# Kernel tuning notes

Measured on AMD Instinct MI355X. Metric: run time of the kernel, lower is better.

Reference implementation:

```python
import jax, jax.numpy as jnp
import numpy as np

H = 16      # attention heads
D = 1024    # embedding size
HD = 64     # head size = D // H


def setup_inputs() -> dict:
    key = jax.random.key(0)
    ks = jax.random.split(key, 6)
    s = 1.0 / np.sqrt(D)
    x = jax.random.normal(ks[0], (2, 2048, D), dtype=jnp.float32)
    Wq = jax.random.normal(ks[1], (H, D, HD), dtype=jnp.float32) * s
    Wk = jax.random.normal(ks[2], (H, D, HD), dtype=jnp.float32) * s
    Wv = jax.random.normal(ks[3], (H, D, HD), dtype=jnp.float32) * s
    Wo = jax.random.normal(ks[4], (H * HD, D), dtype=jnp.float32) * s
    bo = jax.random.normal(ks[5], (D,), dtype=jnp.float32) * 0.01
    return {"x": x, "Wq": Wq, "Wk": Wk, "Wv": Wv, "Wo": Wo, "bo": bo}


def reference(x, Wq, Wk, Wv, Wo, bo):
    # x: [B, S, D]; per-head projections batched over the head axis.
    B, S, _ = x.shape
    q = jnp.einsum('bsd,hde->bhse', x, Wq)  # [B,H,S,HD]
    k = jnp.einsum('bsd,hde->bhse', x, Wk)
    v = jnp.einsum('bsd,hde->bhse', x, Wv)
    scale = 1.0 / jnp.sqrt(jnp.asarray(HD, dtype=x.dtype))
    scores = jnp.einsum('bhqe,bhke->bhqk', q, k) * scale  # [B,H,S,S]
    causal = jnp.tril(jnp.ones((S, S), dtype=bool))
    scores = jnp.where(causal, scores, jnp.asarray(-jnp.inf, dtype=x.dtype))
    attn = jax.nn.softmax(scores, axis=-1)
    out = jnp.einsum('bhqk,bhke->bhqe', attn, v)  # [B,H,S,HD]
    # concat heads along last dim (head order matches ModuleList order)
    out = out.transpose(0, 2, 1, 3).reshape(B, S, H * HD)
    return out @ Wo + bo  # dropout is identity in eval mode
```

## Files before the change

### kernel.cpp

```cpp
#include <hip/hip_runtime.h>
#include <hip/hip_bf16.h>
#include <cstdint>

#define Hh 16
#define Dd 1024
#define HD 64
#define Bb 2
#define Ss 2048

typedef float f32x4 __attribute__((ext_vector_type(4)));
typedef __bf16 bf16x8 __attribute__((ext_vector_type(8)));

__device__ __forceinline__ unsigned short f2bf(float f) {
  union { float f; unsigned u; } v; v.f = f;
  unsigned r = (v.u + 0x7FFFu + ((v.u >> 16) & 1u)) >> 16;
  return (unsigned short)r;
}

__device__ __forceinline__ void gld16(const void* g, void* l) {
  __builtin_amdgcn_global_load_lds(
      (__attribute__((address_space(1))) void*)(g),
      (__attribute__((address_space(3))) void*)(l),
      16, 0, 0);
}

__global__ __launch_bounds__(256)
void pack_x_k(const float4* __restrict__ x, unsigned short* __restrict__ xb, int n4) {
  const int i = blockIdx.x * blockDim.x + threadIdx.x;
  if (i >= n4) return;
  const float4 v = x[i];
  ushort4 o;
  o.x = f2bf(v.x); o.y = f2bf(v.y); o.z = f2bf(v.z); o.w = f2bf(v.w);
  *(ushort4*)&xb[(size_t)i * 4] = o;
}

__global__ __launch_bounds__(256)
void tconv_k(const float* __restrict__ in, unsigned short* __restrict__ out,
             int R, int C, float scale) {
  __shared__ float T[64][65];
  const int m = blockIdx.z;
  const float* src = in + (size_t)m * R * C;
  unsigned short* dst = out + (size_t)m * R * C;
  const int c0 = blockIdx.x * 64, r0 = blockIdx.y * 64;
  const int tx = threadIdx.x & 63, ty = threadIdx.x >> 6;
#pragma unroll
  for (int it = 0; it < 16; ++it) {
    const int i = ty + it * 4;
    T[i][tx] = src[(size_t)(r0 + i) * C + c0 + tx];
  }
  __syncthreads();
#pragma unroll
  for (int it = 0; it < 16; ++it) {
    const int jj = ty + it * 4;
    dst[(size_t)(c0 + jj) * R + r0 + tx] = f2bf(T[tx][jj] * scale);
  }
}

template <int EPI>
__global__ __launch_bounds__(256)
void gemm_bt(const unsigned short* __restrict__ A,
             const unsigned short* __restrict__ Bt,
             int K, int Ndim,
             unsigned short* __restrict__ q_out,
             unsigned short* __restrict__ k_out,
             unsigned short* __restrict__ vt_out,
             float* __restrict__ o_out,
             const float* __restrict__ bias)
{
  __shared__ unsigned short As[128 * 64];
  __shared__ unsigned short Bs[128 * 64];

  const int tid = threadIdx.x;
  const int w = tid >> 6, lane = tid & 63;
  const int lo = lane & 15, hi = lane >> 4;
  const int wr = w >> 1, wc = w & 1;
  const int row0 = blockIdx.y * 128;
  const int col0 = blockIdx.x * 128;

  f32x4 acc[4][4] = {};

  const int er = w * 32 + (lane >> 3);
  const int ec = (lane & 7) * 8;

  for (int k0 = 0; k0 < K; k0 += 64) {
#pragma unroll
    for (int c = 0; c < 4; ++c) {
      const int rr = er + c * 8;
      gld16(A  + (size_t)(row0 + rr) * K + (k0 + ec), (char*)As + (size_t)(w * 4 + c) * 1024);
      gld16(Bt + (size_t)(col0 + rr) * K + (k0 + ec), (char*)Bs + (size_t)(w * 4 + c) * 1024);
    }
    __syncthreads();
#pragma unroll
    for (int ks = 0; ks < 2; ++ks) {
      bf16x8 af[4], bfr[4];
#pragma unroll
      for (int i = 0; i < 4; ++i)
        af[i] = *(const bf16x8*)&As[(wr * 64 + i * 16 + lo) * 64 + ks * 32 + hi * 8];
#pragma unroll
      for (int j = 0; j < 4; ++j)
        bfr[j] = *(const bf16x8*)&Bs[(wc * 64 + j * 16 + lo) * 64 + ks * 32 + hi * 8];
#pragma unroll
      for (int i = 0; i < 4; ++i)
#pragma unroll
        for (int j = 0; j < 4; ++j)
          acc[i][j] = __builtin_amdgcn_mfma_f32_16x16x32_bf16(af[i], bfr[j], acc[i][j], 0, 0, 0);
    }
    __syncthreads();
  }

#pragma unroll
  for (int i = 0; i < 4; ++i) {
    const int grow = row0 + wr * 64 + i * 16 + hi * 4;
#pragma unroll
    for (int j = 0; j < 4; ++j) {
      const int gcol = col0 + wc * 64 + j * 16 + lo;
      if (EPI == 0) {
        const int p  = gcol >> 10;
        const int hd = (gcol >> 6) & 15;
        const int e  = gcol & 63;
        const int bb2 = grow >> 11;
        const int s   = grow & 2047;
        const int bh  = bb2 * Hh + hd;
        if (p == 2) {
          const size_t base = ((size_t)bh * HD + e) * Ss + s;
          ushort4 pk;
          pk.x = f2bf(acc[i][j][0]); pk.y = f2bf(acc[i][j][1]);
          pk.z = f2bf(acc[i][j][2]); pk.w = f2bf(acc[i][j][3]);
          *(ushort4*)&vt_out[base] = pk;
        } else {
          unsigned short* dst = (p == 0) ? q_out : k_out;
          const size_t base = ((size_t)bh * Ss + s) * HD + e;
#pragma unroll
          for (int r = 0; r < 4; ++r) dst[base + (size_t)r * HD] = f2bf(acc[i][j][r]);
        }
      } else {
        const size_t base = (size_t)grow * Ndim + gcol;
        const float bv = bias[gcol];
#pragma unroll
        for (int r = 0; r < 4; ++r) o_out[base + (size_t)r * Ndim] = acc[i][j][r] + bv;
      }
    }
  }
}

__global__ __launch_bounds__(256)
void attn_fwd(const unsigned short* __restrict__ qb,
              const unsigned short* __restrict__ kb,
              const unsigned short* __restrict__ vtb,
              unsigned short* __restrict__ ob)
{
  __shared__ unsigned short Ks[2][64 * 64];
  __shared__ unsigned short Vs[2][64 * 64];
  __shared__ unsigned short Ps[4][16 * 64];

  const int qt = 31 - blockIdx.y;
  const int bh = blockIdx.x;
  const int bb2 = bh >> 4;
  const int hd = bh & 15;

  const unsigned short* Q  = qb  + (size_t)bh * Ss * HD;
  const unsigned short* Kg = kb  + (size_t)bh * Ss * HD;
  const unsigned short* Vt = vtb + (size_t)bh * HD * Ss;

  const int tid = threadIdx.x;
  const int w = tid >> 6, lane = tid & 63;
  const int lo = lane & 15, hi = lane >> 4;
  const int qrow0 = qt * 64 + w * 16;

  const int srow = lane >> 3;
  const int scol = ((lane & 7) ^ (lane >> 3)) * 8;

#define STAGE(bi, kv)                                                     \
  _Pragma("unroll")                                                       \
  for (int c = 0; c < 2; ++c) {                                           \
    const int L = c * 4 + w;                                              \
    const int rr = L * 8 + srow;                                          \
    gld16(Kg + (size_t)((kv) + rr) * HD + scol,                           \
          (char*)&Ks[bi][0] + L * 1024);                                  \
    gld16(Vt + (size_t)rr * Ss + (kv) + scol,                             \
          (char*)&Vs[bi][0] + L * 1024);                                  \
  }

  const int swl = (lo & 7) << 4;

  bf16x8 vones;
#pragma unroll
  for (int j = 0; j < 8; ++j) vones[j] = (__bf16)1.0f;

  bf16x8 qf[2];
#pragma unroll
  for (int ks = 0; ks < 2; ++ks)
    qf[ks] = *(const bf16x8*)&Q[(size_t)(qrow0 + lo) * HD + ks * 32 + hi * 8];

  f32x4 oacc[4] = {};
  float m2[4], l2[4];
#pragma unroll
  for (int r = 0; r < 4; ++r) { m2[r] = -INFINITY; l2[r] = 0.f; }

  const int ntiles = qt + 1;

  STAGE(0, 0);
  __syncthreads();

  int cur = 0;
  for (int t = 0; t < ntiles; ++t) {
    if (t + 1 < ntiles) { STAGE(cur ^ 1, (t + 1) * 64); }

    const int kv0 = t * 64;
    const bool diag = (t == qt);

    f32x4 sacc[4] = {};
    __builtin_amdgcn_s_setprio(1);
#pragma unroll
    for (int ks = 0; ks < 2; ++ks) {
      bf16x8 kf[4];
#pragma unroll
      for (int nj = 0; nj < 4; ++nj)
        kf[nj] = *(const bf16x8*)((const char*)&Ks[cur][0] +
                 (nj * 16 + lo) * 128 + ((ks * 64 + hi * 16) ^ swl));
#pragma unroll
      for (int nj = 0; nj < 4; ++nj)
        sacc[nj] = __builtin_amdgcn_mfma_f32_16x16x32_bf16(qf[ks], kf[nj], sacc[nj], 0, 0, 0);
    }
    __builtin_amdgcn_s_setprio(0);

    float lm[4];
    float dmax = -INFINITY;
#pragma unroll
    for (int r = 0; r < 4; ++r) {
      if (diag) {
        const int q = qrow0 + hi * 4 + r;
#pragma unroll
        for (int nj = 0; nj < 4; ++nj) {
          const int kk = kv0 + nj * 16 + lo;
          if (kk > q) sacc[nj][r] = -INFINITY;
        }
      }
      lm[r] = fmaxf(fmaxf(sacc[0][r], sacc[1][r]), fmaxf(sacc[2][r], sacc[3][r]));
      dmax = fmaxf(dmax, lm[r] - m2[r]);
    }
    if (!__all(dmax <= 8.0f)) {
#pragma unroll
      for (int r = 0; r < 4; ++r) {
        float rm = lm[r];
#pragma unroll
        for (int d = 1; d < 16; d <<= 1)
          rm = fmaxf(rm, __shfl_xor(rm, d, 64));
        const float mn = fmaxf(m2[r], rm);
        const float rc = __builtin_amdgcn_exp2f(m2[r] - mn);
        m2[r] = mn;
        l2[r] *= rc;
#pragma unroll
        for (int nj = 0; nj < 4; ++nj)
          oacc[nj][r] *= rc;
      }
    }

    unsigned short* Pw = &Ps[w][0];
#pragma unroll
    for (int nj = 0; nj < 4; ++nj)
#pragma unroll
      for (int r = 0; r < 4; ++r) {
        const float p = __builtin_amdgcn_exp2f(sacc[nj][r] - m2[r]);
        const int prow = hi * 4 + r;
        const int pcb = (nj * 32 + lo * 2) ^ ((prow & 7) << 4);
        *(__bf16*)((char*)Pw + prow * 128 + pcb) = (__bf16)p;
      }

    f32x4 osum = {};
    __builtin_amdgcn_s_setprio(1);
#pragma unroll
    for (int ks = 0; ks < 2; ++ks) {
      bf16x8 pa, vf[4];
      pa = *(const bf16x8*)((const char*)Pw +
           lo * 128 + ((ks * 64 + hi * 16) ^ swl));
#pragma unroll
      for (int nj = 0; nj < 4; ++nj)
        vf[nj] = *(const bf16x8*)((const char*)&Vs[cur][0] +
                 (nj * 16 + lo) * 128 + ((ks * 64 + hi * 16) ^ swl));
#pragma unroll
      for (int nj = 0; nj < 4; ++nj)
        oacc[nj] = __builtin_amdgcn_mfma_f32_16x16x32_bf16(pa, vf[nj], oacc[nj], 0, 0, 0);
      osum = __builtin_amdgcn_mfma_f32_16x16x32_bf16(pa, vones, osum, 0, 0, 0);
    }
    __builtin_amdgcn_s_setprio(0);
#pragma unroll
    for (int r = 0; r < 4; ++r)
      l2[r] += osum[r];

    __syncthreads();
    cur ^= 1;
  }
#undef STAGE

#pragma unroll
  for (int r = 0; r < 4; ++r) {
    const int s = qrow0 + hi * 4 + r;
    const float il = 1.0f / l2[r];
    const size_t base = ((size_t)bb2 * Ss + s) * Dd + hd * HD;
#pragma unroll
    for (int nj = 0; nj < 4; ++nj)
      ob[base + nj * 16 + lo] = f2bf(oacc[nj][r] * il);
  }
}

extern "C" void kernel_launch(void* const* d_in, const int* in_sizes, int n_in,
                              void* d_out, int out_size, void* d_ws, size_t ws_size,
                              hipStream_t stream)
{
  const float* x  = (const float*)d_in[0];
  const float* Wq = (const float*)d_in[1];
  const float* Wk = (const float*)d_in[2];
  const float* Wv = (const float*)d_in[3];
  const float* Wo = (const float*)d_in[4];
  const float* bo = (const float*)d_in[5];
  float* out = (float*)d_out;

  char* ws = (char*)d_ws;
  unsigned short* xb    = (unsigned short*)(ws);
  unsigned short* wqkvT = (unsigned short*)(ws + 8388608);
  unsigned short* woT   = (unsigned short*)(ws + 14680064);
  unsigned short* qb    = (unsigned short*)(ws + 16777216);
  unsigned short* kb    = (unsigned short*)(ws + 25165824);
  unsigned short* vtb   = (unsigned short*)(ws + 33554432);
  unsigned short* ob    = (unsigned short*)(ws + 41943040);

  pack_x_k<<<4096, 256, 0, stream>>>((const float4*)x, xb, 1048576);
  tconv_k<<<dim3(1, 16, 16), 256, 0, stream>>>(Wq, wqkvT,           1024, 64, 0.18033688011112042f);
  tconv_k<<<dim3(1, 16, 16), 256, 0, stream>>>(Wk, wqkvT + 1048576, 1024, 64, 1.0f);
  tconv_k<<<dim3(1, 16, 16), 256, 0, stream>>>(Wv, wqkvT + 2097152, 1024, 64, 1.0f);
  tconv_k<<<dim3(16, 16, 1), 256, 0, stream>>>(Wo, woT,             1024, 1024, 1.0f);

  gemm_bt<0><<<dim3(24, 32), 256, 0, stream>>>(xb, wqkvT, 1024, 3072,
                                               qb, kb, vtb, nullptr, nullptr);
  attn_fwd<<<dim3(32, 32), 256, 0, stream>>>(qb, kb, vtb, ob);
  gemm_bt<1><<<dim3(8, 32), 256, 0, stream>>>(ob, woT, 1024, 1024,
                                              nullptr, nullptr, nullptr, out, bo);
}
```

Before: 140.3 us.

## Double-buffer GEMM LDS tiles with swizzle and vectorize transposed epilogue stores

The GEMM now double-buffers its A/B LDS tiles, issuing the next tile's async global-to-LDS loads before computing the current one. It adds an XOR swizzle to cut LDS bank conflicts and raises wave priority around the MFMA block. For Q/K and the output projection it swaps the MFMA operand order so each lane holds four consecutive columns, allowing packed ushort4/float4 stores instead of scalar strided stores. The V projection moves to its own launch that keeps the transposed layout, so the QKV GEMM becomes two kernels, and doubling LDS may lower occupancy.

```diff
diff --git a/kernel.cpp b/kernel.cpp
--- a/kernel.cpp
+++ b/kernel.cpp
@@ -67,8 +67,8 @@
              float* __restrict__ o_out,
              const float* __restrict__ bias)
 {
-  __shared__ unsigned short As[128 * 64];
-  __shared__ unsigned short Bs[128 * 64];
+  __shared__ unsigned short As[2][128 * 64];
+  __shared__ unsigned short Bs[2][128 * 64];
 
   const int tid = threadIdx.x;
   const int w = tid >> 6, lane = tid & 63;
@@ -79,68 +79,91 @@
 
   f32x4 acc[4][4] = {};
 
-  const int er = w * 32 + (lane >> 3);
-  const int ec = (lane & 7) * 8;
-
-  for (int k0 = 0; k0 < K; k0 += 64) {
-#pragma unroll
-    for (int c = 0; c < 4; ++c) {
-      const int rr = er + c * 8;
-      gld16(A  + (size_t)(row0 + rr) * K + (k0 + ec), (char*)As + (size_t)(w * 4 + c) * 1024);
-      gld16(Bt + (size_t)(col0 + rr) * K + (k0 + ec), (char*)Bs + (size_t)(w * 4 + c) * 1024);
-    }
-    __syncthreads();
+  const int srow = w * 32 + (lane >> 3);
+  const int scol = ((lane & 7) ^ (lane >> 3)) * 8;
+  const int swl  = (lo & 7) << 4;
+
+#define GSTAGE(bi, k0)                                                    \
+  _Pragma("unroll")                                                       \
+  for (int c = 0; c < 4; ++c) {                                           \
+    const int rr = srow + c * 8;                                          \
+    gld16(A  + (size_t)(row0 + rr) * K + ((k0) + scol),                   \
+          (char*)&As[bi][0] + (w * 4 + c) * 1024);                        \
+    gld16(Bt + (size_t)(col0 + rr) * K + ((k0) + scol),                   \
+          (char*)&Bs[bi][0] + (w * 4 + c) * 1024);                        \
+  }
+
+  GSTAGE(0, 0);
+  __syncthreads();
+
+  const int nst = K >> 6;
+  int cur = 0;
+  for (int t = 0; t < nst; ++t) {
+    if (t + 1 < nst) { GSTAGE(cur ^ 1, (t + 1) * 64); }
 #pragma unroll
     for (int ks = 0; ks < 2; ++ks) {
       bf16x8 af[4], bfr[4];
 #pragma unroll
       for (int i = 0; i < 4; ++i)
-        af[i] = *(const bf16x8*)&As[(wr * 64 + i * 16 + lo) * 64 + ks * 32 + hi * 8];
+        af[i] = *(const bf16x8*)((const char*)&As[cur][0] +
+                 (wr * 64 + i * 16 + lo) * 128 + ((ks * 64 + hi * 16) ^ swl));
 #pragma unroll
       for (int j = 0; j < 4; ++j)
-        bfr[j] = *(const bf16x8*)&Bs[(wc * 64 + j * 16 + lo) * 64 + ks * 32 + hi * 8];
+        bfr[j] = *(const bf16x8*)((const char*)&Bs[cur][0] +
+                 (wc * 64 + j * 16 + lo) * 128 + ((ks * 64 + hi * 16) ^ swl));
+      __builtin_amdgcn_s_setprio(1);
 #pragma unroll
       for (int i = 0; i < 4; ++i)
 #pragma unroll
-        for (int j = 0; j < 4; ++j)
-          acc[i][j] = __builtin_amdgcn_mfma_f32_16x16x32_bf16(af[i], bfr[j], acc[i][j], 0, 0, 0);
+        for (int j = 0; j < 4; ++j) {
+          if (EPI == 1)
+            acc[i][j] = __builtin_amdgcn_mfma_f32_16x16x32_bf16(af[i], bfr[j], acc[i][j], 0, 0, 0);
+          else
+            acc[i][j] = __builtin_amdgcn_mfma_f32_16x16x32_bf16(bfr[j], af[i], acc[i][j], 0, 0, 0);
+        }
+      __builtin_amdgcn_s_setprio(0);
     }
     __syncthreads();
+    cur ^= 1;
   }
 
 #pragma unroll
   for (int i = 0; i < 4; ++i) {
-    const int grow = row0 + wr * 64 + i * 16 + hi * 4;
 #pragma unroll
     for (int j = 0; j < 4; ++j) {
-      const int gcol = col0 + wc * 64 + j * 16 + lo;
-      if (EPI == 0) {
-        const int p  = gcol >> 10;
-        const int hd = (gcol >> 6) & 15;
-        const int e  = gcol & 63;
-        const int bb2 = grow >> 11;
-        const int s   = grow & 2047;
-        const int bh  = bb2 * Hh + hd;
-        if (p == 2) {
-          const size_t base = ((size_t)bh * HD + e) * Ss + s;
+      if (EPI == 1) {
+        const int grow = row0 + wr * 64 + i * 16 + hi * 4;
+        const int gcol = col0 + wc * 64 + j * 16 + lo;
+        const int hd = gcol >> 6, e = gcol & 63;
+        const int bb2 = grow >> 11, s = grow & 2047;
+        ushort4 pk;
+        pk.x = f2bf(acc[i][j][0]); pk.y = f2bf(acc[i][j][1]);
+        pk.z = f2bf(acc[i][j][2]); pk.w = f2bf(acc[i][j][3]);
+        *(ushort4*)&vt_out[((size_t)(bb2 * Hh + hd) * HD + e) * Ss + s] = pk;
+      } else {
+        const int m  = row0 + wr * 64 + i * 16 + lo;
+        const int n0 = col0 + wc * 64 + j * 16 + hi * 4;
+        if (EPI == 0) {
+          const int p = n0 >> 10;
+          const int hd = (n0 >> 6) & 15;
+          const int e = n0 & 63;
+          const int bb2 = m >> 11, s = m & 2047;
+          unsigned short* dst = (p == 0) ? q_out : k_out;
           ushort4 pk;
           pk.x = f2bf(acc[i][j][0]); pk.y = f2bf(acc[i][j][1]);
           pk.z = f2bf(acc[i][j][2]); pk.w = f2bf(acc[i][j][3]);
-          *(ushort4*)&vt_out[base] = pk;
+          *(ushort4*)&dst[((size_t)(bb2 * Hh + hd) * Ss + s) * HD + e] = pk;
         } else {
-          unsigned short* dst = (p == 0) ? q_out : k_out;
-          const size_t base = ((size_t)bh * Ss + s) * HD + e;
-#pragma unroll
-          for (int r = 0; r < 4; ++r) dst[base + (size_t)r * HD] = f2bf(acc[i][j][r]);
+          const float4 bv = *(const float4*)&bias[n0];
+          float4 o;
+          o.x = acc[i][j][0] + bv.x; o.y = acc[i][j][1] + bv.y;
+          o.z = acc[i][j][2] + bv.z; o.w = acc[i][j][3] + bv.w;
+          *(float4*)&o_out[(size_t)m * Ndim + n0] = o;
         }
-      } else {
-        const size_t base = (size_t)grow * Ndim + gcol;
-        const float bv = bias[gcol];
-#pragma unroll
-        for (int r = 0; r < 4; ++r) o_out[base + (size_t)r * Ndim] = acc[i][j][r] + bv;
       }
     }
   }
+#undef GSTAGE
 }
 
 __global__ __launch_bounds__(256)
@@ -331,9 +354,11 @@
   tconv_k<<<dim3(1, 16, 16), 256, 0, stream>>>(Wv, wqkvT + 2097152, 1024, 64, 1.0f);
   tconv_k<<<dim3(16, 16, 1), 256, 0, stream>>>(Wo, woT,             1024, 1024, 1.0f);
 
-  gemm_bt<0><<<dim3(24, 32), 256, 0, stream>>>(xb, wqkvT, 1024, 3072,
-                                               qb, kb, vtb, nullptr, nullptr);
+  gemm_bt<0><<<dim3(16, 32), 256, 0, stream>>>(xb, wqkvT, 1024, 0,
+                                               qb, kb, nullptr, nullptr, nullptr);
+  gemm_bt<1><<<dim3(8, 32), 256, 0, stream>>>(xb, wqkvT + 2097152, 1024, 0,
+                                              nullptr, nullptr, vtb, nullptr, nullptr);
   attn_fwd<<<dim3(32, 32), 256, 0, stream>>>(qb, kb, vtb, ob);
-  gemm_bt<1><<<dim3(8, 32), 256, 0, stream>>>(ob, woT, 1024, 1024,
+  gemm_bt<2><<<dim3(8, 32), 256, 0, stream>>>(ob, woT, 1024, 1024,
                                               nullptr, nullptr, nullptr, out, bo);
 }
```

Measured after the change: 131.0 us. 6.6% less time.
